# Optimization experiments

Hardware: AMD Instinct MI355X
Metric: run time of the kernel (lower is better)

The kernel has to match this reference:

```python
import jax, jax.numpy as jnp
import numpy as np

S, B, D = 2048, 2, 1024
H, DH = 16, 64  # heads, dim_head; H*DH == D (required by out.view)
SCALE = DH ** -0.5


def setup_inputs() -> dict:
    key = jax.random.key(0)
    ks = jax.random.split(key, 9)
    s = 0.02
    return {
        "x": jax.random.normal(ks[0], (S, B, D), jnp.float32),
        "Wq": jax.random.normal(ks[1], (H * DH, D), jnp.float32) * s,
        "bq": jax.random.normal(ks[2], (H * DH,), jnp.float32) * s,
        "Wk": jax.random.normal(ks[3], (H * DH, D), jnp.float32) * s,
        "bk": jax.random.normal(ks[4], (H * DH,), jnp.float32) * s,
        "Wv": jax.random.normal(ks[5], (H * DH, D), jnp.float32) * s,
        "bv": jax.random.normal(ks[6], (H * DH,), jnp.float32) * s,
        "Wo": jax.random.normal(ks[7], (D, H * DH), jnp.float32) * s,
        "bo": jax.random.normal(ks[8], (D,), jnp.float32) * s,
    }


def reference(x, Wq, bq, Wk, bk, Wv, bv, Wo, bo):
    # x: [S, B, D] (seq-first, matching the torch module)
    q = (x @ Wq.T + bq).reshape(S, B, H, DH)
    k = (x @ Wk.T + bk).reshape(S, B, H, DH)
    v = (x @ Wv.T + bv).reshape(S, B, H, DH)
    # scores: [B, H, S, S]
    dots = jnp.einsum("sbhd,tbhd->bhst", q, k) * SCALE
    attn = jax.nn.softmax(dots, axis=-1)  # dropout p=0.0 -> identity
    out = jnp.einsum("bhst,tbhd->sbhd", attn, v).reshape(S, B, H * DH)
    return out @ Wo.T + bo
```

## Files before the change

kernel.cpp:

```cpp
#include <hip/hip_runtime.h>
#include <hip/hip_bf16.h>

typedef unsigned short u16;
typedef unsigned int u32;
typedef __bf16 bf16x8 __attribute__((ext_vector_type(8)));
typedef float f32x4 __attribute__((ext_vector_type(4)));
typedef float f32x16 __attribute__((ext_vector_type(16)));

static constexpr int kS = 2048;
static constexpr int kB = 2;
static constexpr int kD = 1024;
static constexpr int kDH = 64;
static constexpr int kM = kS * kB;
static constexpr float kScale = 0.125f;
static constexpr float kLog2e = 1.44269504088896340736f;

__device__ __forceinline__ u16 f2bf(float f) {
  return __builtin_bit_cast(u16, static_cast<__bf16>(f));
}

__device__ __forceinline__ u32 pack2(float lo, float hi) {
  union { u16 h[2]; u32 u; } x;
  x.h[0] = f2bf(lo); x.h[1] = f2bf(hi);
  return x.u;
}

__device__ __forceinline__ void permswap(u32& a, u32& b) {
  asm volatile("v_permlane32_swap_b32 %0, %1" : "+v"(a), "+v"(b));
}

__device__ __forceinline__ float exp2_hw(float x) {
  float r;
  asm("v_exp_f32 %0, %1" : "=v"(r) : "v"(x));
  return r;
}

__device__ __forceinline__ void load_lds16(const void* g, void* l) {
  __builtin_amdgcn_global_load_lds(
      (const __attribute__((address_space(1))) void*)g,
      (__attribute__((address_space(3))) void*)l, 16, 0, 0);
}

__global__ void cast_all(const float* __restrict__ x,
                         const float* __restrict__ Wq, const float* __restrict__ Wk,
                         const float* __restrict__ Wv, const float* __restrict__ Wo,
                         u16* __restrict__ xb,
                         u16* __restrict__ dq, u16* __restrict__ dk,
                         u16* __restrict__ dv, u16* __restrict__ dw) {
  const int bid = blockIdx.x;
  const float* src; u16* dst; int i;
  if (bid < 4096) {
    src = x; dst = xb;
    i = (bid * 256 + (int)threadIdx.x) * 4;
  } else {
    const int r = bid - 4096;
    switch (r >> 10) {
      case 0: src = Wq; dst = dq; break;
      case 1: src = Wk; dst = dk; break;
      case 2: src = Wv; dst = dv; break;
      default: src = Wo; dst = dw; break;
    }
    i = ((r & 1023) * 256 + (int)threadIdx.x) * 4;
  }
  const float4 v = *reinterpret_cast<const float4*>(src + i);
  ushort4 o;
  o.x = f2bf(v.x); o.y = f2bf(v.y); o.z = f2bf(v.z); o.w = f2bf(v.w);
  *reinterpret_cast<ushort4*>(dst + i) = o;
}

template <int MODE>
__device__ __forceinline__ void gemm_body(
    const u16* __restrict__ A, const u16* __restrict__ W,
    const float* __restrict__ bias, void* __restrict__ Out,
    int M, int N, int K, float oscale) {
  __shared__ u16 As[128 * 64];
  __shared__ u16 Bs[128 * 64];
  const int tid = threadIdx.x;
  const int lane = tid & 63;
  const int wid = tid >> 6;
  const int wr = (wid >> 2) * 64;
  const int wc = (wid & 3) * 32;
  const int l15 = lane & 15;
  const int lg = lane >> 4;
  const int tm = blockIdx.x * 128;
  const int tn = blockIdx.y * 128;

  auto stage = [&](int k0) {
#pragma unroll
    for (int p = 0; p < 2; ++p) {
      const int c = p * 512 + tid;
      const int row = c >> 3;
      const int scc = (c & 7) ^ (row & 7);
      load_lds16(A + (size_t)(tm + row) * K + k0 + scc * 8, &As[c * 8]);
      load_lds16(W + (size_t)(tn + row) * K + k0 + scc * 8, &Bs[c * 8]);
    }
  };

  f32x4 acc[4][2] = {};

#pragma unroll 1
  for (int ks = 0; ks < K / 64; ++ks) {
    stage(ks * 64);
    __syncthreads();
#pragma unroll
    for (int kh = 0; kh < 2; ++kh) {
      bf16x8 af[4], bw[2];
#pragma unroll
      for (int i = 0; i < 4; ++i) {
        const int row = wr + i * 16 + l15;
        af[i] = *reinterpret_cast<const bf16x8*>(
            &As[row * 64 + (((kh * 4 + lg) ^ (row & 7)) * 8)]);
      }
#pragma unroll
      for (int j = 0; j < 2; ++j) {
        const int row = wc + j * 16 + l15;
        bw[j] = *reinterpret_cast<const bf16x8*>(
            &Bs[row * 64 + (((kh * 4 + lg) ^ (row & 7)) * 8)]);
      }
#pragma unroll
      for (int i = 0; i < 4; ++i)
#pragma unroll
        for (int j = 0; j < 2; ++j)
          acc[i][j] = __builtin_amdgcn_mfma_f32_16x16x32_bf16(af[i], bw[j], acc[i][j], 0, 0, 0);
    }
    __syncthreads();
  }

#pragma unroll
  for (int i = 0; i < 4; ++i)
#pragma unroll
    for (int j = 0; j < 2; ++j)
#pragma unroll
      for (int r = 0; r < 4; ++r) {
        const int row = tm + wr + i * 16 + lg * 4 + r;
        const int col = tn + wc + j * 16 + l15;
        const float v = (acc[i][j][r] + bias[col]) * oscale;
        if constexpr (MODE == 0) {
          reinterpret_cast<u16*>(Out)[(size_t)row * N + col] = f2bf(v);
        } else if constexpr (MODE == 1) {
          reinterpret_cast<float*>(Out)[(size_t)row * N + col] = v;
        } else {
          const int s_ = row >> 1, b_ = row & 1;
          const int h_ = col >> 6, dh_ = col & 63;
          reinterpret_cast<u16*>(Out)[((size_t)(b_ * 16 + h_) * 64 + dh_) * kS + s_] = f2bf(v);
        }
      }
}

__global__ __launch_bounds__(512, 6) void qkv_gemm(
    const u16* __restrict__ xb,
    const u16* __restrict__ Wqb, const u16* __restrict__ Wkb, const u16* __restrict__ Wvb,
    const float* __restrict__ bq, const float* __restrict__ bk, const float* __restrict__ bv,
    u16* __restrict__ Q, u16* __restrict__ K, u16* __restrict__ Vt) {
  const int z = blockIdx.z;
  if (z == 2) {
    gemm_body<2>(xb, Wvb, bv, Vt, kM, kD, kD, 1.0f);
  } else if (z == 0) {
    gemm_body<0>(xb, Wqb, bq, Q, kM, kD, kD, kScale * kLog2e);
  } else {
    gemm_body<0>(xb, Wkb, bk, K, kM, kD, kD, 1.0f);
  }
}

__global__ __launch_bounds__(512, 6) void out_gemm(
    const u16* __restrict__ Ob, const u16* __restrict__ Wob,
    const float* __restrict__ bo, float* __restrict__ out) {
  gemm_body<1>(Ob, Wob, bo, out, kM, kD, kD, 1.0f);
}

__global__ __launch_bounds__(512, 4) void attn_fwd(
    const u16* __restrict__ Qg, const u16* __restrict__ Kg,
    const u16* __restrict__ Vtg, u16* __restrict__ Og) {
  __shared__ u16 Ksm[2 * 4096];
  __shared__ u16 Vsm[2 * 2 * 4096];

  const int tid = threadIdx.x;
  const int lane = tid & 63;
  const int w = tid >> 6;
  const int half = w >> 2;
  const int wsub = w & 3;
  const int ltid = tid & 255;
  const int l31 = lane & 31;
  const int hi = lane >> 5;

  const int bid = blockIdx.x;
  const int xcd = bid & 7;
  const int idx = bid >> 3;
  const int bh = xcd * 4 + (idx & 3);
  const int qb = idx >> 2;
  const int b = bh & 1;
  const int h = bh >> 1;
  const int hoff = h * kDH;
  const int vslot = b * 16 + h;
  const int qrow = qb * 128 + wsub * 32 + l31;

  u16* Kh = &Ksm[half * 4096];
  u16* Vh = &Vsm[half * 2 * 4096];

  bf16x8 qf[4];
#pragma unroll
  for (int ks = 0; ks < 4; ++ks)
    qf[ks] = *reinterpret_cast<const bf16x8*>(
        &Qg[(size_t)(qrow * kB + b) * kD + hoff + ks * 16 + hi * 8]);

  f32x16 acc[2] = {};
  float lac[4] = {0.f, 0.f, 0.f, 0.f};

  auto stage = [&](int t0, int vbuf) {
#pragma unroll
    for (int p = 0; p < 2; ++p) {
      const int c = p * 256 + ltid;
      const int row = c >> 3;
      const int scc = (c & 7) ^ (row & 7);
      load_lds16(&Kg[(size_t)((t0 + row) * kB + b) * kD + hoff + scc * 8],
                 &Kh[c * 8]);
      load_lds16(&Vtg[(size_t)(vslot * 64 + row) * kS + t0 + scc * 8],
                 &Vh[vbuf * 4096 + c * 8]);
    }
  };

  const int tbase = half * 16;
  stage(tbase * 64, 0);

#pragma unroll 1
  for (int ti = 0; ti < 16; ++ti) {
    asm volatile("s_waitcnt vmcnt(0)" ::: "memory");
    __builtin_amdgcn_sched_barrier(0);
    __builtin_amdgcn_s_barrier();
    __builtin_amdgcn_sched_barrier(0);

    f32x16 sc[2] = {};
    __builtin_amdgcn_s_setprio(1);
#pragma unroll
    for (int nb = 0; nb < 2; ++nb) {
      const int krow = nb * 32 + l31;
#pragma unroll
      for (int ks = 0; ks < 4; ++ks) {
        const bf16x8 kf = *reinterpret_cast<const bf16x8*>(
            &Kh[krow * 64 + (((ks * 2 + hi) ^ (krow & 7)) * 8)]);
        sc[nb] = __builtin_amdgcn_mfma_f32_32x32x16_bf16(kf, qf[ks], sc[nb], 0, 0, 0);
      }
    }
    __builtin_amdgcn_s_setprio(0);

    __builtin_amdgcn_sched_barrier(0);
    __builtin_amdgcn_s_barrier();
    __builtin_amdgcn_sched_barrier(0);
    if (ti + 1 < 16) stage((tbase + ti + 1) * 64, (ti + 1) & 1);

    const int cur = ti & 1;

    bf16x8 pb[4];
#pragma unroll
    for (int nb = 0; nb < 2; ++nb) {
      float p[16];
#pragma unroll
      for (int r = 0; r < 16; ++r) {
        p[r] = exp2_hw(sc[nb][r]);
        lac[r & 3] += p[r];
      }
      u32 pk[4][2];
#pragma unroll
      for (int q = 0; q < 4; ++q)
#pragma unroll
        for (int w2 = 0; w2 < 2; ++w2)
          pk[q][w2] = pack2(p[4 * q + 2 * w2], p[4 * q + 2 * w2 + 1]);
#pragma unroll
      for (int k1 = 0; k1 < 2; ++k1) {
        u32 a0 = pk[2 * k1][0], b0 = pk[2 * k1 + 1][0];
        u32 a1 = pk[2 * k1][1], b1 = pk[2 * k1 + 1][1];
        permswap(a0, b0);
        permswap(a1, b1);
        union { u32 wv[4]; bf16x8 v; } U;
        U.wv[0] = a0; U.wv[1] = a1; U.wv[2] = b0; U.wv[3] = b1;
        pb[2 * nb + k1] = U.v;
      }
    }

    __builtin_amdgcn_s_setprio(1);
#pragma unroll
    for (int ks = 0; ks < 4; ++ks)
#pragma unroll
      for (int n2 = 0; n2 < 2; ++n2) {
        const int vrow = n2 * 32 + l31;
        const bf16x8 va = *reinterpret_cast<const bf16x8*>(
            &Vh[cur * 4096 + vrow * 64 + (((ks * 2 + hi) ^ (vrow & 7)) * 8)]);
        acc[n2] = __builtin_amdgcn_mfma_f32_32x32x16_bf16(va, pb[ks], acc[n2], 0, 0, 0);
      }
    __builtin_amdgcn_s_setprio(0);
  }

  __syncthreads();
  float* Ocmb = reinterpret_cast<float*>(&Vsm[0]);
  float* Lcmb = reinterpret_cast<float*>(&Ksm[0]);
  const float l_own = (lac[0] + lac[1]) + (lac[2] + lac[3]);
  const float l_half = l_own + __shfl_xor(l_own, 32);
  const int q = wsub * 32 + l31;

  if (half == 1) {
    if (hi == 0) Lcmb[q] = l_half;
#pragma unroll
    for (int n2 = 0; n2 < 2; ++n2)
#pragma unroll
      for (int q4 = 0; q4 < 4; ++q4)
#pragma unroll
        for (int rp = 0; rp < 2; ++rp) {
          const int dh0 = n2 * 32 + q4 * 8 + hi * 4 + rp * 2;
          const int a = q * 64 + (dh0 ^ ((l31 & 7) << 3));
          *reinterpret_cast<float2*>(&Ocmb[a]) =
              make_float2(acc[n2][q4 * 4 + rp * 2], acc[n2][q4 * 4 + rp * 2 + 1]);
        }
  }
  __syncthreads();
  if (half == 0) {
    const float inv = 1.0f / (l_half + Lcmb[q]);
#pragma unroll
    for (int n2 = 0; n2 < 2; ++n2)
#pragma unroll
      for (int q4 = 0; q4 < 4; ++q4)
#pragma unroll
        for (int rp = 0; rp < 2; ++rp) {
          const int dh0 = n2 * 32 + q4 * 8 + hi * 4 + rp * 2;
          const int a = q * 64 + (dh0 ^ ((l31 & 7) << 3));
          const float2 o = *reinterpret_cast<const float2*>(&Ocmb[a]);
          acc[n2][q4 * 4 + rp * 2]     += o.x;
          acc[n2][q4 * 4 + rp * 2 + 1] += o.y;
        }
#pragma unroll
    for (int n2 = 0; n2 < 2; ++n2)
#pragma unroll
      for (int g = 0; g < 4; ++g) {
        const int dh0 = n2 * 32 + g * 8 + hi * 4;
        ushort4 o;
        o.x = f2bf(acc[n2][g * 4 + 0] * inv);
        o.y = f2bf(acc[n2][g * 4 + 1] * inv);
        o.z = f2bf(acc[n2][g * 4 + 2] * inv);
        o.w = f2bf(acc[n2][g * 4 + 3] * inv);
        *reinterpret_cast<ushort4*>(&Og[(size_t)(qrow * kB + b) * kD + hoff + dh0]) = o;
      }
  }
}

extern "C" void kernel_launch(void* const* d_in, const int* in_sizes, int n_in,
                              void* d_out, int out_size, void* d_ws, size_t ws_size,
                              hipStream_t stream) {
  const float* x  = (const float*)d_in[0];
  const float* Wq = (const float*)d_in[1];
  const float* bq = (const float*)d_in[2];
  const float* Wk = (const float*)d_in[3];
  const float* bk = (const float*)d_in[4];
  const float* Wv = (const float*)d_in[5];
  const float* bv = (const float*)d_in[6];
  const float* Wo = (const float*)d_in[7];
  const float* bo = (const float*)d_in[8];
  float* out = (float*)d_out;

  char* ws = (char*)d_ws;
  u16* xb  = (u16*)(ws + 0);
  u16* Wqb = (u16*)(ws + 8388608);
  u16* Wkb = (u16*)(ws + 10485760);
  u16* Wvb = (u16*)(ws + 12582912);
  u16* Wob = (u16*)(ws + 14680064);
  u16* Qb  = (u16*)(ws + 16777216);
  u16* Kb  = (u16*)(ws + 25165824);
  u16* Vtb = (u16*)(ws + 33554432);
  u16* Ob  = (u16*)(ws + 41943040);

  cast_all<<<8192, 256, 0, stream>>>(x, Wq, Wk, Wv, Wo, xb, Wqb, Wkb, Wvb, Wob);

  qkv_gemm<<<dim3(kM / 128, kD / 128, 3), 512, 0, stream>>>(
      xb, Wqb, Wkb, Wvb, bq, bk, bv, Qb, Kb, Vtb);

  attn_fwd<<<512, 512, 0, stream>>>(Qb, Kb, Vtb, Ob);

  out_gemm<<<dim3(kM / 128, kD / 128), 512, 0, stream>>>(Ob, Wob, bo, out);
}
```

Measured before the change: 115.2 us.

## Double-buffer GEMM LDS tiles and shrink N tile to 64

Reworks the shared GEMM body so the next K-slice is prefetched into a second LDS buffer while MFMAs run on the current one, with a single barrier per iteration in place of two. The N tile drops from 128 to 64 and each wave now computes a 32x32 sub-tile, which doubles the grid for the QKV and output projections. The aim is to hide global-to-LDS latency and fill more CUs. The cost is less arithmetic per loaded A tile, more LDS per block, and a lower occupancy hint in the launch bounds.

```diff
diff --git a/kernel.cpp b/kernel.cpp
--- a/kernel.cpp
+++ b/kernel.cpp
@@ -73,61 +73,74 @@
     const u16* __restrict__ A, const u16* __restrict__ W,
     const float* __restrict__ bias, void* __restrict__ Out,
     int M, int N, int K, float oscale) {
-  __shared__ u16 As[128 * 64];
-  __shared__ u16 Bs[128 * 64];
+  __shared__ u16 As[2][128 * 64];
+  __shared__ u16 Bs[2][64 * 64];
   const int tid = threadIdx.x;
   const int lane = tid & 63;
   const int wid = tid >> 6;
-  const int wr = (wid >> 2) * 64;
-  const int wc = (wid & 3) * 32;
+  const int wr = (wid >> 1) * 32;
+  const int wc = (wid & 1) * 32;
   const int l15 = lane & 15;
   const int lg = lane >> 4;
   const int tm = blockIdx.x * 128;
-  const int tn = blockIdx.y * 128;
-
-  auto stage = [&](int k0) {
-#pragma unroll
-    for (int p = 0; p < 2; ++p) {
+  const int tn = blockIdx.y * 64;
+
+  auto stage = [&](int k0, int buf) {
+#pragma unroll
+    for (int p = 0; p < 3; ++p) {
       const int c = p * 512 + tid;
-      const int row = c >> 3;
-      const int scc = (c & 7) ^ (row & 7);
-      load_lds16(A + (size_t)(tm + row) * K + k0 + scc * 8, &As[c * 8]);
-      load_lds16(W + (size_t)(tn + row) * K + k0 + scc * 8, &Bs[c * 8]);
+      if (c < 1024) {
+        const int row = c >> 3;
+        const int scc = (c & 7) ^ (row & 7);
+        load_lds16(A + (size_t)(tm + row) * K + k0 + scc * 8, &As[buf][c * 8]);
+      } else {
+        const int cb = c - 1024;
+        const int row = cb >> 3;
+        const int scc = (cb & 7) ^ (row & 7);
+        load_lds16(W + (size_t)(tn + row) * K + k0 + scc * 8, &Bs[buf][cb * 8]);
+      }
     }
   };
 
-  f32x4 acc[4][2] = {};
+  f32x4 acc[2][2] = {};
+  const int nsteps = K / 64;
+
+  stage(0, 0);
 
 #pragma unroll 1
-  for (int ks = 0; ks < K / 64; ++ks) {
-    stage(ks * 64);
-    __syncthreads();
+  for (int ks = 0; ks < nsteps; ++ks) {
+    asm volatile("s_waitcnt vmcnt(0)" ::: "memory");
+    __builtin_amdgcn_sched_barrier(0);
+    __builtin_amdgcn_s_barrier();
+    __builtin_amdgcn_sched_barrier(0);
+    const int cur = ks & 1;
+    if (ks + 1 < nsteps) stage((ks + 1) * 64, cur ^ 1);
+
 #pragma unroll
     for (int kh = 0; kh < 2; ++kh) {
-      bf16x8 af[4], bw[2];
-#pragma unroll
-      for (int i = 0; i < 4; ++i) {
+      bf16x8 af[2], bw[2];
+#pragma unroll
+      for (int i = 0; i < 2; ++i) {
         const int row = wr + i * 16 + l15;
         af[i] = *reinterpret_cast<const bf16x8*>(
-            &As[row * 64 + (((kh * 4 + lg) ^ (row & 7)) * 8)]);
+            &As[cur][row * 64 + (((kh * 4 + lg) ^ (row & 7)) * 8)]);
       }
 #pragma unroll
       for (int j = 0; j < 2; ++j) {
         const int row = wc + j * 16 + l15;
         bw[j] = *reinterpret_cast<const bf16x8*>(
-            &Bs[row * 64 + (((kh * 4 + lg) ^ (row & 7)) * 8)]);
-      }
-#pragma unroll
-      for (int i = 0; i < 4; ++i)
+            &Bs[cur][row * 64 + (((kh * 4 + lg) ^ (row & 7)) * 8)]);
+      }
+#pragma unroll
+      for (int i = 0; i < 2; ++i)
 #pragma unroll
         for (int j = 0; j < 2; ++j)
           acc[i][j] = __builtin_amdgcn_mfma_f32_16x16x32_bf16(af[i], bw[j], acc[i][j], 0, 0, 0);
     }
-    __syncthreads();
-  }
-
-#pragma unroll
-  for (int i = 0; i < 4; ++i)
+  }
+
+#pragma unroll
+  for (int i = 0; i < 2; ++i)
 #pragma unroll
     for (int j = 0; j < 2; ++j)
 #pragma unroll
@@ -147,7 +160,7 @@
       }
 }
 
-__global__ __launch_bounds__(512, 6) void qkv_gemm(
+__global__ __launch_bounds__(512, 4) void qkv_gemm(
     const u16* __restrict__ xb,
     const u16* __restrict__ Wqb, const u16* __restrict__ Wkb, const u16* __restrict__ Wvb,
     const float* __restrict__ bq, const float* __restrict__ bk, const float* __restrict__ bv,
@@ -162,7 +175,7 @@
   }
 }
 
-__global__ __launch_bounds__(512, 6) void out_gemm(
+__global__ __launch_bounds__(512, 4) void out_gemm(
     const u16* __restrict__ Ob, const u16* __restrict__ Wob,
     const float* __restrict__ bo, float* __restrict__ out) {
   gemm_body<1>(Ob, Wob, bo, out, kM, kD, kD, 1.0f);
@@ -368,10 +381,10 @@
 
   cast_all<<<8192, 256, 0, stream>>>(x, Wq, Wk, Wv, Wo, xb, Wqb, Wkb, Wvb, Wob);
 
-  qkv_gemm<<<dim3(kM / 128, kD / 128, 3), 512, 0, stream>>>(
+  qkv_gemm<<<dim3(kM / 128, kD / 64, 3), 512, 0, stream>>>(
       xb, Wqb, Wkb, Wvb, bq, bk, bv, Qb, Kb, Vtb);
 
   attn_fwd<<<512, 512, 0, stream>>>(Qb, Kb, Vtb, Ob);
 
-  out_gemm<<<dim3(kM / 128, kD / 128), 512, 0, stream>>>(Ob, Wob, bo, out);
-}
+  out_gemm<<<dim3(kM / 128, kD / 64), 512, 0, stream>>>(Ob, Wob, bo, out);
+}
```

After: 150.5 us. +30.6%, slower.
